# Kernel tuning notes

Hardware: AMD Instinct MI355X
Metric: run time of the kernel (lower is better)

Reference implementation:

```python
import jax, jax.numpy as jnp
import numpy as np

B, S, E, H = 4, 2048, 2048, 16
D = E // H  # head_dim = 128


def setup_inputs() -> dict:
    key = jax.random.key(0)
    ks = jax.random.split(key, 10)
    sc = 1.0 / np.sqrt(E)
    x = jax.random.normal(ks[0], (B, S, E), dtype=jnp.float32)
    causal_mask = jnp.tril(jnp.ones((S, S), dtype=jnp.int32))  # 1 = keep, 0 = mask
    wq = jax.random.normal(ks[1], (E, E), dtype=jnp.float32) * sc
    bq = jax.random.normal(ks[2], (E,), dtype=jnp.float32) * sc
    wk = jax.random.normal(ks[3], (E, E), dtype=jnp.float32) * sc
    bk = jax.random.normal(ks[4], (E,), dtype=jnp.float32) * sc
    wv = jax.random.normal(ks[5], (E, E), dtype=jnp.float32) * sc
    bv = jax.random.normal(ks[6], (E,), dtype=jnp.float32) * sc
    wo = jax.random.normal(ks[7], (E, E), dtype=jnp.float32) * sc
    bo = jax.random.normal(ks[8], (E,), dtype=jnp.float32) * sc
    return {"x": x, "causal_mask": causal_mask, "wq": wq, "bq": bq,
            "wk": wk, "bk": bk, "wv": wv, "bv": bv, "wo": wo, "bo": bo}


def _split_heads(t):
    # [B,S,E] -> [B,H,S,D]
    return t.reshape(B, S, H, D).transpose(0, 2, 1, 3)


def reference(x, causal_mask, wq, bq, wk, bk, wv, bv, wo, bo):
    # torch Linear: y = x @ W.T + b
    q = _split_heads(x @ wq.T + bq)
    k = _split_heads(x @ wk.T + bk)
    v = _split_heads(x @ wv.T + bv)
    scale = 1.0 / jnp.sqrt(jnp.asarray(D, dtype=x.dtype))
    dots = jnp.einsum("bhqd,bhkd->bhqk", q, k) * scale
    dots = jnp.where(causal_mask == 0, jnp.asarray(-jnp.inf, dots.dtype), dots)
    attn = jax.nn.softmax(dots, axis=-1)
    ctx = jnp.einsum("bhqk,bhkd->bhqd", attn, v)
    ctx = ctx.transpose(0, 2, 1, 3).reshape(B, S, E)  # merge heads
    return ctx @ wo.T + bo
```

## Files before the change

kernel.cpp:

```cpp
#include <hip/hip_runtime.h>
#include <hip/hip_bf16.h>

#define B_ 4
#define S_ 2048
#define E_ 2048
#define H_ 16
#define D_ 128
#define M_ (B_*S_)

typedef __attribute__((ext_vector_type(8))) short short8;
typedef __attribute__((ext_vector_type(4))) float f32x4;

__device__ __forceinline__ unsigned short f2bf(float f) {
  union { __hip_bfloat16 h; unsigned short u; } c;
  c.h = __float2bfloat16(f);
  return c.u;
}

__device__ __forceinline__ void gld_lds16(const void* g, void* l) {
  __builtin_amdgcn_global_load_lds((const __attribute__((address_space(1))) void*)g,
                                   (__attribute__((address_space(3))) void*)l, 16, 0, 0);
}

__device__ __forceinline__ float fexp2(float x) {
#if __has_builtin(__builtin_amdgcn_exp2f)
  return __builtin_amdgcn_exp2f(x);
#else
  return exp2f(x);
#endif
}

__global__ __launch_bounds__(256) void cast_bf16_kernel(const float* __restrict__ in,
                                                        unsigned short* __restrict__ out,
                                                        int n4) {
  int i = blockIdx.x * 256 + threadIdx.x;
  if (i >= n4) return;
  float4 v = ((const float4*)in)[i];
  ushort4 o;
  o.x = f2bf(v.x); o.y = f2bf(v.y); o.z = f2bf(v.z); o.w = f2bf(v.w);
  ((ushort4*)out)[i] = o;
}

__global__ __launch_bounds__(256) void cast_w4_kernel(const float* __restrict__ w0,
                                                      const float* __restrict__ w1,
                                                      const float* __restrict__ w2,
                                                      const float* __restrict__ w3,
                                                      unsigned short* __restrict__ o0,
                                                      unsigned short* __restrict__ o1,
                                                      unsigned short* __restrict__ o2,
                                                      unsigned short* __restrict__ o3,
                                                      int n4) {
  int i = blockIdx.x * 256 + threadIdx.x;
  if (i >= n4) return;
  const float* in = (blockIdx.y == 0) ? w0 : (blockIdx.y == 1) ? w1 : (blockIdx.y == 2) ? w2 : w3;
  unsigned short* out = (blockIdx.y == 0) ? o0 : (blockIdx.y == 1) ? o1 : (blockIdx.y == 2) ? o2 : o3;
  float4 v = ((const float4*)in)[i];
  ushort4 o;
  o.x = f2bf(v.x); o.y = f2bf(v.y); o.z = f2bf(v.z); o.w = f2bf(v.w);
  ((ushort4*)out)[i] = o;
}

template <typename OutT, bool TR>
__device__ __forceinline__ void gemm_core(const unsigned short* __restrict__ A,
                                          const unsigned short* __restrict__ W,
                                          const float* __restrict__ bias,
                                          OutT* __restrict__ C,
                                          int M, int N, int K, float oscale,
                                          int m0, int n0,
                                          unsigned short* As, unsigned short* Bs) {
  const int tid  = threadIdx.x;
  const int lane = tid & 63;
  const int wid  = tid >> 6;
  const int wr = (wid >> 2) * 128;
  const int wc = (wid & 3) * 64;
  const int lr  = lane & 15;
  const int lg  = lane >> 4;

  f32x4 acc[8][4];
#pragma unroll
  for (int i = 0; i < 8; i++)
#pragma unroll
    for (int j = 0; j < 4; j++) acc[i][j] = (f32x4){0.f, 0.f, 0.f, 0.f};

  const int rS = tid >> 3;
  const int uS = (tid & 7) ^ (rS & 7);
  const unsigned short* asrc = A + (size_t)(m0 + rS) * K + uS * 8;
  const unsigned short* bsrc = W + (size_t)(n0 + rS) * K + uS * 8;
  char* adst = (char*)As + wid * 1024;
  char* bdst = (char*)Bs + wid * 1024;

  const int swR = (lr & 7) << 4;
  const int nK = K >> 6;

#pragma unroll
  for (int i = 0; i < 4; ++i) {
    gld_lds16(asrc + (size_t)(64 * i) * K, adst + i * 8192);
    gld_lds16(bsrc + (size_t)(64 * i) * K, bdst + i * 8192);
  }

  for (int t = 0; t < nK; ++t) {
    const int bo = (t & 1) * 32768;
    __syncthreads();

    if (t + 1 < nK) {
      const int kt2 = (t + 1) * 64;
      const int nbo = bo ^ 32768;
#pragma unroll
      for (int i = 0; i < 4; ++i) {
        gld_lds16(asrc + kt2 + (size_t)(64 * i) * K, adst + nbo + i * 8192);
        gld_lds16(bsrc + kt2 + (size_t)(64 * i) * K, bdst + nbo + i * 8192);
      }
    }

    const char* AsB = (const char*)As + bo;
    const char* BsB = (const char*)Bs + bo;
#pragma unroll
    for (int kk = 0; kk < 2; kk++) {
      const int cb = ((kk * 4 + lg) << 4) ^ swR;
      short8 bf[4];
#pragma unroll
      for (int j = 0; j < 4; j++)
        bf[j] = *(const short8*)(BsB + (wc + j * 16 + lr) * 128 + cb);
#pragma unroll
      for (int mh = 0; mh < 2; mh++) {
        short8 af[4];
#pragma unroll
        for (int i = 0; i < 4; i++)
          af[i] = *(const short8*)(AsB + (wr + mh * 64 + i * 16 + lr) * 128 + cb);
        __builtin_amdgcn_s_setprio(1);
#pragma unroll
        for (int i = 0; i < 4; i++)
#pragma unroll
          for (int j = 0; j < 4; j++) {
            if constexpr (TR)
              acc[mh * 4 + i][j] = __builtin_amdgcn_mfma_f32_16x16x32_bf16(bf[j], af[i], acc[mh * 4 + i][j], 0, 0, 0);
            else
              acc[mh * 4 + i][j] = __builtin_amdgcn_mfma_f32_16x16x32_bf16(af[i], bf[j], acc[mh * 4 + i][j], 0, 0, 0);
          }
        __builtin_amdgcn_s_setprio(0);
      }
    }
  }

  if constexpr (TR) {
    const int lg4 = lg * 4;
#pragma unroll
    for (int j = 0; j < 4; j++) {
      const int gn = n0 + wc + j * 16 + lg4;
      const float4 bv4 = *(const float4*)&bias[gn];
#pragma unroll
      for (int i = 0; i < 8; i++) {
        const int gm = m0 + wr + i * 16 + lr;
#pragma unroll
        for (int r = 0; r < 4; r++) {
          const float v = (acc[i][j][r] + ((const float*)&bv4)[r]) * oscale;
          ((unsigned short*)C)[(size_t)(gn + r) * M + gm] = f2bf(v);
        }
      }
    }
  } else {
#pragma unroll
    for (int i = 0; i < 8; i++) {
      const int gm = m0 + wr + i * 16 + lg * 4;
#pragma unroll
      for (int j = 0; j < 4; j++) {
        const int gn = n0 + wc + j * 16 + lr;
        const float bv = bias[gn];
#pragma unroll
        for (int r = 0; r < 4; r++) {
          const float v = (acc[i][j][r] + bv) * oscale;
          if constexpr (sizeof(OutT) == 2)
            ((unsigned short*)C)[(size_t)(gm + r) * N + gn] = f2bf(v);
          else
            ((float*)C)[(size_t)(gm + r) * N + gn] = v;
        }
      }
    }
  }
}

template <typename OutT, bool TR = false>
__global__ __launch_bounds__(512) void gemm_bt256(const unsigned short* __restrict__ A,
                                                  const unsigned short* __restrict__ W,
                                                  const float* __restrict__ bias,
                                                  OutT* __restrict__ C,
                                                  int M, int N, int K, float oscale) {
  __shared__ unsigned short As[2 * 256 * 64];
  __shared__ unsigned short Bs[2 * 256 * 64];
  const int nwg = gridDim.x * gridDim.y;
  const int lin = blockIdx.x + gridDim.x * blockIdx.y;
  const int nl  = (lin & 7) * (nwg >> 3) + (lin >> 3);
  const int m0 = (nl / gridDim.x) * 256;
  const int n0 = (nl % gridDim.x) * 256;
  gemm_core<OutT, TR>(A, W, bias, C, M, N, K, oscale, m0, n0, As, Bs);
}

__global__ __launch_bounds__(256, 2) void flash_attn(const unsigned short* __restrict__ Q,
                                                     const unsigned short* __restrict__ K,
                                                     const unsigned short* __restrict__ VT,
                                                     unsigned short* __restrict__ Ctx) {
  __shared__ unsigned short Ks[64 * 128];
  __shared__ unsigned short Vt[128 * 64];
  __shared__ unsigned short Pl[4 * 2048];

  const int tid  = threadIdx.x;
  const int lane = tid & 63;
  const int wid  = tid >> 6;
  const int lr  = lane & 15;
  const int lg  = lane >> 4;
  const int lk8 = lg * 8;
  const int lin = blockIdx.x + 8 * blockIdx.y + 128 * blockIdx.z;
  const int nl  = (lin & 7) * 64 + (lin >> 3);
  const int bxw = nl & 7;
  const int h   = (nl >> 3) & 15;
  const int b   = nl >> 7;
  const size_t base = ((size_t)b * S_) * E_ + (size_t)h * D_;
  const unsigned short* __restrict__ Kh = K + base;
  const unsigned short* __restrict__ VTh = VT + (size_t)(h * D_) * M_ + (size_t)b * S_;
  unsigned short* Plf = Pl + wid * 2048;

  const int rK = tid >> 4;
  const int cK = ((tid * 16) & 255) ^ ((rK & 7) << 4);
  const unsigned short* ksrcB = Kh + (size_t)rK * E_ + (cK >> 1);
  char* kdstB = (char*)Ks + wid * 1024;

  const int dVb = tid >> 3;
  const int cV  = tid & 7;
  const unsigned short* vsrcB = VTh + (size_t)dVb * M_ + (size_t)((cV ^ (dVb & 7)) * 8);
  char* vdstB = (char*)Vt + wid * 1024;

  const int plw0 = (lg >> 1) * 128 + lr * 8 + (lg & 1) * 4;
  const int plrd = lg * 128 + lr * 8;

#pragma unroll 1
  for (int half = 0; half < 2; ++half) {
    const int ti = half ? (15 - bxw) : bxw;
    const int qblk = ti * 128;
    const int qrow0 = qblk + wid * 16 + lr;
    const int qrow1 = qrow0 + 64;

    short8 qf0[4], qf1[4];
#pragma unroll
    for (int kk = 0; kk < 4; kk++) {
      qf0[kk] = *(const short8*)&Q[base + (size_t)qrow0 * E_ + kk * 32 + lk8];
      qf1[kk] = *(const short8*)&Q[base + (size_t)qrow1 * E_ + kk * 32 + lk8];
    }

    f32x4 o0[8], o1[8];
#pragma unroll
    for (int d0 = 0; d0 < 8; d0++) {
      o0[d0] = (f32x4){0.f, 0.f, 0.f, 0.f};
      o1[d0] = (f32x4){0.f, 0.f, 0.f, 0.f};
    }
    float m0r = -INFINITY, m1r = -INFINITY;
    float l0 = 0.f, l1 = 0.f;

    const int nt = 2 * ti + 2;

    for (int t = 0; t < nt; ++t) {
      const int kv0 = t * 64;
      const size_t koff = (size_t)kv0 * E_;

#pragma unroll
      for (int p = 0; p < 4; ++p) {
        gld_lds16(ksrcB + koff + (size_t)(16 * p) * E_, kdstB + p * 4096);
        gld_lds16(vsrcB + (size_t)(32 * p) * M_ + kv0,  vdstB + p * 4096);
      }
      __syncthreads();

      const bool g0act = (t < nt - 1);
      const bool mk0   = (t == nt - 2);
      const bool mk1   = (t == nt - 1);

      f32x4 s0[4], s1[4];
#pragma unroll
      for (int c = 0; c < 4; c++) {
        s0[c] = (f32x4){0.f, 0.f, 0.f, 0.f};
        s1[c] = (f32x4){0.f, 0.f, 0.f, 0.f};
      }
      const int swK = (lr & 7) << 4;
      if (g0act) {
        __builtin_amdgcn_s_setprio(1);
#pragma unroll
        for (int kk = 0; kk < 4; kk++) {
          const int cb = (kk * 64 + lg * 16) ^ swK;
#pragma unroll
          for (int c = 0; c < 4; c++) {
            const short8 kf = *(const short8*)((const char*)Ks + (c * 16 + lr) * 256 + cb);
            s1[c] = __builtin_amdgcn_mfma_f32_16x16x32_bf16(kf, qf1[kk], s1[c], 0, 0, 0);
            s0[c] = __builtin_amdgcn_mfma_f32_16x16x32_bf16(kf, qf0[kk], s0[c], 0, 0, 0);
          }
        }
        __builtin_amdgcn_s_setprio(0);
      } else {
        __builtin_amdgcn_s_setprio(1);
#pragma unroll
        for (int kk = 0; kk < 4; kk++) {
          const int cb = (kk * 64 + lg * 16) ^ swK;
#pragma unroll
          for (int c = 0; c < 4; c++) {
            const short8 kf = *(const short8*)((const char*)Ks + (c * 16 + lr) * 256 + cb);
            s1[c] = __builtin_amdgcn_mfma_f32_16x16x32_bf16(kf, qf1[kk], s1[c], 0, 0, 0);
          }
        }
        __builtin_amdgcn_s_setprio(0);
      }

      {
        float v[4][4];
#pragma unroll
        for (int c = 0; c < 4; c++)
#pragma unroll
          for (int r = 0; r < 4; r++) v[c][r] = s1[c][r];
        if (mk1) {
#pragma unroll
          for (int c = 0; c < 4; c++) {
            const int kvq = kv0 + c * 16 + lg * 4;
#pragma unroll
            for (int r = 0; r < 4; r++)
              if (kvq + r > qrow1) v[c][r] = -INFINITY;
          }
        }
        float pm = fmaxf(fmaxf(fmaxf(v[0][0], v[0][1]), fmaxf(v[0][2], v[0][3])),
                         fmaxf(fmaxf(v[1][0], v[1][1]), fmaxf(v[1][2], v[1][3])));
        pm = fmaxf(pm, fmaxf(fmaxf(fmaxf(v[2][0], v[2][1]), fmaxf(v[2][2], v[2][3])),
                             fmaxf(fmaxf(v[3][0], v[3][1]), fmaxf(v[3][2], v[3][3]))));
        pm = fmaxf(pm, __shfl_xor(pm, 16));
        pm = fmaxf(pm, __shfl_xor(pm, 32));
        const float need = pm - m1r;
        if (!__all(need <= 8.f)) {
          const float mnew = fmaxf(m1r, pm);
          const float al = fexp2(m1r - mnew);
          l1 *= al;
#pragma unroll
          for (int d0 = 0; d0 < 8; ++d0) {
            f32x4 tt = o1[d0];
            tt[0] *= al; tt[1] *= al; tt[2] *= al; tt[3] *= al;
            o1[d0] = tt;
          }
          m1r = mnew;
        }
        ushort4 wpk[4];
        float ps = 0.f;
#pragma unroll
        for (int c = 0; c < 4; c++) {
          const float e0 = fexp2(v[c][0] - m1r);
          const float e1 = fexp2(v[c][1] - m1r);
          const float e2 = fexp2(v[c][2] - m1r);
          const float e3 = fexp2(v[c][3] - m1r);
          wpk[c].x = f2bf(e0); wpk[c].y = f2bf(e1);
          wpk[c].z = f2bf(e2); wpk[c].w = f2bf(e3);
          ps += (e0 + e1) + (e2 + e3);
        }
        l1 += ps;
#pragma unroll
        for (int c = 0; c < 4; c++)
          *(ushort4*)&Plf[1024 + plw0 + c * 256] = wpk[c];
      }

      if (g0act) {
        float v[4][4];
#pragma unroll
        for (int c = 0; c < 4; c++)
#pragma unroll
          for (int r = 0; r < 4; r++) v[c][r] = s0[c][r];
        if (mk0) {
#pragma unroll
          for (int c = 0; c < 4; c++) {
            const int kvq = kv0 + c * 16 + lg * 4;
#pragma unroll
            for (int r = 0; r < 4; r++)
              if (kvq + r > qrow0) v[c][r] = -INFINITY;
          }
        }
        float pm = fmaxf(fmaxf(fmaxf(v[0][0], v[0][1]), fmaxf(v[0][2], v[0][3])),
                         fmaxf(fmaxf(v[1][0], v[1][1]), fmaxf(v[1][2], v[1][3])));
        pm = fmaxf(pm, fmaxf(fmaxf(fmaxf(v[2][0], v[2][1]), fmaxf(v[2][2], v[2][3])),
                             fmaxf(fmaxf(v[3][0], v[3][1]), fmaxf(v[3][2], v[3][3]))));
        pm = fmaxf(pm, __shfl_xor(pm, 16));
        pm = fmaxf(pm, __shfl_xor(pm, 32));
        const float need = pm - m0r;
        if (!__all(need <= 8.f)) {
          const float mnew = fmaxf(m0r, pm);
          const float al = fexp2(m0r - mnew);
          l0 *= al;
#pragma unroll
          for (int d0 = 0; d0 < 8; ++d0) {
            f32x4 tt = o0[d0];
            tt[0] *= al; tt[1] *= al; tt[2] *= al; tt[3] *= al;
            o0[d0] = tt;
          }
          m0r = mnew;
        }
        ushort4 wpk[4];
        float ps = 0.f;
#pragma unroll
        for (int c = 0; c < 4; c++) {
          const float e0 = fexp2(v[c][0] - m0r);
          const float e1 = fexp2(v[c][1] - m0r);
          const float e2 = fexp2(v[c][2] - m0r);
          const float e3 = fexp2(v[c][3] - m0r);
          wpk[c].x = f2bf(e0); wpk[c].y = f2bf(e1);
          wpk[c].z = f2bf(e2); wpk[c].w = f2bf(e3);
          ps += (e0 + e1) + (e2 + e3);
        }
        l0 += ps;
#pragma unroll
        for (int c = 0; c < 4; c++)
          *(ushort4*)&Plf[plw0 + c * 256] = wpk[c];
      }

      asm volatile("s_waitcnt lgkmcnt(0)" ::: "memory");
      __builtin_amdgcn_sched_barrier(0);

      const short8 pb1a = *(const short8*)&Plf[1024 + plrd];
      const short8 pb1b = *(const short8*)&Plf[1024 + plrd + 512];
      const int d7 = lr & 7;
      if (g0act) {
        const short8 pb0a = *(const short8*)&Plf[plrd];
        const short8 pb0b = *(const short8*)&Plf[plrd + 512];
        __builtin_amdgcn_s_setprio(1);
#pragma unroll
        for (int d0 = 0; d0 < 8; ++d0) {
          const int d = d0 * 16 + lr;
          const short8 vb0 = *(const short8*)&Vt[d * 64 + ((lg ^ d7) << 3)];
          const short8 vb1 = *(const short8*)&Vt[d * 64 + (((4 + lg) ^ d7) << 3)];
          o1[d0] = __builtin_amdgcn_mfma_f32_16x16x32_bf16(vb0, pb1a, o1[d0], 0, 0, 0);
          o1[d0] = __builtin_amdgcn_mfma_f32_16x16x32_bf16(vb1, pb1b, o1[d0], 0, 0, 0);
          o0[d0] = __builtin_amdgcn_mfma_f32_16x16x32_bf16(vb0, pb0a, o0[d0], 0, 0, 0);
          o0[d0] = __builtin_amdgcn_mfma_f32_16x16x32_bf16(vb1, pb0b, o0[d0], 0, 0, 0);
        }
        __builtin_amdgcn_s_setprio(0);
      } else {
        __builtin_amdgcn_s_setprio(1);
#pragma unroll
        for (int d0 = 0; d0 < 8; ++d0) {
          const int d = d0 * 16 + lr;
          const short8 vb0 = *(const short8*)&Vt[d * 64 + ((lg ^ d7) << 3)];
          const short8 vb1 = *(const short8*)&Vt[d * 64 + (((4 + lg) ^ d7) << 3)];
          o1[d0] = __builtin_amdgcn_mfma_f32_16x16x32_bf16(vb0, pb1a, o1[d0], 0, 0, 0);
          o1[d0] = __builtin_amdgcn_mfma_f32_16x16x32_bf16(vb1, pb1b, o1[d0], 0, 0, 0);
        }
        __builtin_amdgcn_s_setprio(0);
      }
      __syncthreads();
    }

    float ls0 = l0, ls1 = l1;
    ls0 += __shfl_xor(ls0, 16); ls0 += __shfl_xor(ls0, 32);
    ls1 += __shfl_xor(ls1, 16); ls1 += __shfl_xor(ls1, 32);
    const float inv0 = 1.0f / ls0;
    const float inv1 = 1.0f / ls1;
    unsigned short* crow0 = Ctx + base + (size_t)qrow0 * E_ + lg * 4;
    unsigned short* crow1 = Ctx + base + (size_t)qrow1 * E_ + lg * 4;
#pragma unroll
    for (int d0 = 0; d0 < 8; ++d0) {
      ushort4 st0, st1;
      st0.x = f2bf(o0[d0][0] * inv0);
      st0.y = f2bf(o0[d0][1] * inv0);
      st0.z = f2bf(o0[d0][2] * inv0);
      st0.w = f2bf(o0[d0][3] * inv0);
      st1.x = f2bf(o1[d0][0] * inv1);
      st1.y = f2bf(o1[d0][1] * inv1);
      st1.z = f2bf(o1[d0][2] * inv1);
      st1.w = f2bf(o1[d0][3] * inv1);
      *(ushort4*)&crow0[d0 * 16] = st0;
      *(ushort4*)&crow1[d0 * 16] = st1;
    }
  }
}

extern "C" void kernel_launch(void* const* d_in, const int* in_sizes, int n_in,
                              void* d_out, int out_size, void* d_ws, size_t ws_size,
                              hipStream_t stream) {
  const float* x  = (const float*)d_in[0];
  const float* wq = (const float*)d_in[2];
  const float* bq = (const float*)d_in[3];
  const float* wk = (const float*)d_in[4];
  const float* bk = (const float*)d_in[5];
  const float* wv = (const float*)d_in[6];
  const float* bv = (const float*)d_in[7];
  const float* wo = (const float*)d_in[8];
  const float* bo = (const float*)d_in[9];
  float* out = (float*)d_out;

  char* ws = (char*)d_ws;
  const size_t MB = 1024 * 1024;
  unsigned short* xb  = (unsigned short*)(ws);
  unsigned short* wqb = (unsigned short*)(ws + 32 * MB);
  unsigned short* wkb = (unsigned short*)(ws + 40 * MB);
  unsigned short* wvb = (unsigned short*)(ws + 48 * MB);
  unsigned short* wob = (unsigned short*)(ws + 56 * MB);
  unsigned short* Qb  = (unsigned short*)(ws + 64 * MB);
  unsigned short* Kb  = (unsigned short*)(ws + 96 * MB);
  unsigned short* VTb = (unsigned short*)(ws + 128 * MB);
  unsigned short* Cb  = (unsigned short*)(ws + 160 * MB);

  const int nx4 = M_ * E_ / 4;
  const int nw4 = E_ * E_ / 4;
  cast_bf16_kernel<<<nx4 / 256, 256, 0, stream>>>(x, xb, nx4);
  cast_w4_kernel<<<dim3(nw4 / 256, 4), 256, 0, stream>>>(wq, wk, wv, wo,
                                                         wqb, wkb, wvb, wob, nw4);

  const float scale = 0.08838834764831845f * 1.44269504088896340736f;

  dim3 gg(E_ / 256, M_ / 256);
  gemm_bt256<unsigned short><<<gg, 512, 0, stream>>>(xb, wqb, bq, Qb, M_, E_, E_, scale);
  gemm_bt256<unsigned short><<<gg, 512, 0, stream>>>(xb, wkb, bk, Kb, M_, E_, E_, 1.0f);
  gemm_bt256<unsigned short, true><<<gg, 512, 0, stream>>>(xb, wvb, bv, VTb, M_, E_, E_, 1.0f);

  flash_attn<<<dim3(S_ / 128 / 2, H_, B_), 256, 0, stream>>>(Qb, Kb, VTb, Cb);

  gemm_bt256<float><<<gg, 512, 0, stream>>>(Cb, wob, bo, out, M_, E_, E_, 1.0f);
}
```

Measured before the change: 405.2 us.

## Use four-stage K=32 LDS pipeline with explicit vmcnt waits in GEMM

Replaces the double-buffered K=64 tile loop of the 256x256 GEMM with a four-buffer ring of K=32 slices. Three slices are prefetched ahead and readiness is tracked with explicit s_waitcnt vmcnt counts plus a raw barrier, so global-to-LDS loads overlap MFMA work for longer. The LDS swizzle is changed to suit 64-byte rows. Each barrier now covers half the MFMA work it did before, and correctness relies on the vmcnt arithmetic and the ring-buffer reuse distance staying in step.

```diff
diff --git a/kernel.cpp b/kernel.cpp
--- a/kernel.cpp
+++ b/kernel.cpp
@@ -82,65 +82,67 @@
 #pragma unroll
     for (int j = 0; j < 4; j++) acc[i][j] = (f32x4){0.f, 0.f, 0.f, 0.f};
 
-  const int rS = tid >> 3;
-  const int uS = (tid & 7) ^ (rS & 7);
-  const unsigned short* asrc = A + (size_t)(m0 + rS) * K + uS * 8;
-  const unsigned short* bsrc = W + (size_t)(n0 + rS) * K + uS * 8;
+  const int rSt = tid >> 2;
+  const int uSt = (tid & 3) ^ ((rSt >> 1) & 3);
+  const unsigned short* asrc = A + (size_t)(m0 + rSt) * K + uSt * 8;
+  const unsigned short* bsrc = W + (size_t)(n0 + rSt) * K + uSt * 8;
   char* adst = (char*)As + wid * 1024;
   char* bdst = (char*)Bs + wid * 1024;
-
-  const int swR = (lr & 7) << 4;
-  const int nK = K >> 6;
-
-#pragma unroll
-  for (int i = 0; i < 4; ++i) {
-    gld_lds16(asrc + (size_t)(64 * i) * K, adst + i * 8192);
-    gld_lds16(bsrc + (size_t)(64 * i) * K, bdst + i * 8192);
+  const size_t rowK128 = (size_t)128 * K;
+
+  const int cbq = ((lg ^ ((lr >> 1) & 3)) << 4);
+  const int nT = K >> 5;
+
+  auto STAGE = [&](int s) {
+    const int sb = (s & 3) * 16384;
+    const size_t ko = (size_t)s << 5;
+    gld_lds16(asrc + ko,           adst + sb);
+    gld_lds16(asrc + ko + rowK128, adst + sb + 8192);
+    gld_lds16(bsrc + ko,           bdst + sb);
+    gld_lds16(bsrc + ko + rowK128, bdst + sb + 8192);
+  };
+
+  auto COMPUTE = [&](int t) {
+    const char* AsB = (const char*)As + (t & 3) * 16384;
+    const char* BsB = (const char*)Bs + (t & 3) * 16384;
+    short8 bf[4];
+#pragma unroll
+    for (int j = 0; j < 4; j++)
+      bf[j] = *(const short8*)(BsB + (wc + j * 16 + lr) * 64 + cbq);
+#pragma unroll
+    for (int mh = 0; mh < 2; mh++) {
+      short8 af[4];
+#pragma unroll
+      for (int i = 0; i < 4; i++)
+        af[i] = *(const short8*)(AsB + (wr + mh * 64 + i * 16 + lr) * 64 + cbq);
+      __builtin_amdgcn_s_setprio(1);
+#pragma unroll
+      for (int i = 0; i < 4; i++)
+#pragma unroll
+        for (int j = 0; j < 4; j++) {
+          if constexpr (TR)
+            acc[mh * 4 + i][j] = __builtin_amdgcn_mfma_f32_16x16x32_bf16(bf[j], af[i], acc[mh * 4 + i][j], 0, 0, 0);
+          else
+            acc[mh * 4 + i][j] = __builtin_amdgcn_mfma_f32_16x16x32_bf16(af[i], bf[j], acc[mh * 4 + i][j], 0, 0, 0);
+        }
+      __builtin_amdgcn_s_setprio(0);
+    }
+  };
+
+  STAGE(0); STAGE(1); STAGE(2);
+
+  for (int t = 0; t < nT - 2; ++t) {
+    asm volatile("s_waitcnt vmcnt(8)" ::: "memory");
+    __builtin_amdgcn_s_barrier();
+    if (t + 3 < nT) STAGE(t + 3);
+    COMPUTE(t);
   }
-
-  for (int t = 0; t < nK; ++t) {
-    const int bo = (t & 1) * 32768;
-    __syncthreads();
-
-    if (t + 1 < nK) {
-      const int kt2 = (t + 1) * 64;
-      const int nbo = bo ^ 32768;
-#pragma unroll
-      for (int i = 0; i < 4; ++i) {
-        gld_lds16(asrc + kt2 + (size_t)(64 * i) * K, adst + nbo + i * 8192);
-        gld_lds16(bsrc + kt2 + (size_t)(64 * i) * K, bdst + nbo + i * 8192);
-      }
-    }
-
-    const char* AsB = (const char*)As + bo;
-    const char* BsB = (const char*)Bs + bo;
-#pragma unroll
-    for (int kk = 0; kk < 2; kk++) {
-      const int cb = ((kk * 4 + lg) << 4) ^ swR;
-      short8 bf[4];
-#pragma unroll
-      for (int j = 0; j < 4; j++)
-        bf[j] = *(const short8*)(BsB + (wc + j * 16 + lr) * 128 + cb);
-#pragma unroll
-      for (int mh = 0; mh < 2; mh++) {
-        short8 af[4];
-#pragma unroll
-        for (int i = 0; i < 4; i++)
-          af[i] = *(const short8*)(AsB + (wr + mh * 64 + i * 16 + lr) * 128 + cb);
-        __builtin_amdgcn_s_setprio(1);
-#pragma unroll
-        for (int i = 0; i < 4; i++)
-#pragma unroll
-          for (int j = 0; j < 4; j++) {
-            if constexpr (TR)
-              acc[mh * 4 + i][j] = __builtin_amdgcn_mfma_f32_16x16x32_bf16(bf[j], af[i], acc[mh * 4 + i][j], 0, 0, 0);
-            else
-              acc[mh * 4 + i][j] = __builtin_amdgcn_mfma_f32_16x16x32_bf16(af[i], bf[j], acc[mh * 4 + i][j], 0, 0, 0);
-          }
-        __builtin_amdgcn_s_setprio(0);
-      }
-    }
-  }
+  asm volatile("s_waitcnt vmcnt(4)" ::: "memory");
+  __builtin_amdgcn_s_barrier();
+  COMPUTE(nT - 2);
+  asm volatile("s_waitcnt vmcnt(0)" ::: "memory");
+  __builtin_amdgcn_s_barrier();
+  COMPUTE(nT - 1);
 
   if constexpr (TR) {
     const int lg4 = lg * 4;
@@ -185,8 +187,8 @@
                                                   const float* __restrict__ bias,
                                                   OutT* __restrict__ C,
                                                   int M, int N, int K, float oscale) {
-  __shared__ unsigned short As[2 * 256 * 64];
-  __shared__ unsigned short Bs[2 * 256 * 64];
+  __shared__ unsigned short As[4 * 256 * 32];
+  __shared__ unsigned short Bs[4 * 256 * 32];
   const int nwg = gridDim.x * gridDim.y;
   const int lin = blockIdx.x + gridDim.x * blockIdx.y;
   const int nl  = (lin & 7) * (nwg >> 3) + (lin >> 3);
```

Result: slower. 465.7 us (+14.9%).
